# Performance work log

Measured on AMD Instinct MI355X. Metric: run time of the kernel, lower is better.

The kernel has to match this reference:

```python
import jax, jax.numpy as jnp
import numpy as np
from jax import lax

DN = ('NCHW', 'OIHW', 'NCHW')


def _conv_block(x, w, g, b, pool):
    # 3x3 conv (pad 1), BN-inference folded to affine (g, b), ReLU, optional 2x2 maxpool
    x = lax.conv_general_dilated(x, w, (1, 1), 'SAME', dimension_numbers=DN)
    x = jax.nn.relu(x * g[None, :, None, None] + b[None, :, None, None])
    if pool:
        x = lax.reduce_window(x, -jnp.inf, lax.max, (1, 1, 2, 2), (1, 1, 2, 2), 'VALID')
    return x


def _encode(x, w1, g1, b1, w2, g2, b2, w3, g3, b3, w4, g4, b4):
    # Conv64F: pool in blocks 1,2 (84->42->21), no pool in blocks 3,4; then global avg pool
    x = _conv_block(x, w1, g1, b1, True)
    x = _conv_block(x, w2, g2, b2, True)
    x = _conv_block(x, w3, g3, b3, False)
    x = _conv_block(x, w4, g4, b4, False)
    return jnp.mean(x, axis=(2, 3))  # (N, 64)


def setup_inputs() -> dict:
    key = jax.random.key(0)
    ks = jax.random.split(key, 9)
    B, NQ, Way, Shot, C, H, W = 4, 15, 5, 5, 3, 84, 84
    d = {
        'query': jax.random.normal(ks[0], (B, NQ, C, H, W), jnp.float32),
        'support': jax.random.normal(ks[1], (B, Way, Shot, C, H, W), jnp.float32),
        'w1': jax.random.normal(ks[2], (64, 3, 3, 3), jnp.float32) * 0.1,
        'g1': jnp.ones((64,), jnp.float32), 'b1': jnp.zeros((64,), jnp.float32),
        'w2': jax.random.normal(ks[3], (64, 64, 3, 3), jnp.float32) * 0.05,
        'g2': jnp.ones((64,), jnp.float32), 'b2': jnp.zeros((64,), jnp.float32),
        'w3': jax.random.normal(ks[4], (64, 64, 3, 3), jnp.float32) * 0.05,
        'g3': jnp.ones((64,), jnp.float32), 'b3': jnp.zeros((64,), jnp.float32),
        'w4': jax.random.normal(ks[5], (64, 64, 3, 3), jnp.float32) * 0.05,
        'g4': jnp.ones((64,), jnp.float32), 'b4': jnp.zeros((64,), jnp.float32),
        'fc1_w': jax.random.normal(ks[6], (64, 64), jnp.float32) * 0.1,
        'fc1_b': jnp.zeros((64,), jnp.float32),
        'fc2_w': jax.random.normal(ks[7], (32, 64), jnp.float32) * 0.1,
        'fc2_b': jnp.zeros((32,), jnp.float32),
        'fc3_w': jax.random.normal(ks[8], (1, 32), jnp.float32) * 0.1,
        'fc3_b': jnp.zeros((1,), jnp.float32),
    }
    return d


def reference(query, support, w1, g1, b1, w2, g2, b2, w3, g3, b3, w4, g4, b4,
              fc1_w, fc1_b, fc2_w, fc2_b, fc3_w, fc3_b):
    B, NQ, C, H, W = query.shape
    _, Way, Shot = support.shape[:3]
    enc = lambda x: _encode(x, w1, g1, b1, w2, g2, b2, w3, g3, b3, w4, g4, b4)
    q_emb = enc(query.reshape(-1, C, H, W)).reshape(B, NQ, 64)
    s_emb = enc(support.reshape(-1, C, H, W)).reshape(B, Way, Shot, 64)
    # batched pairwise |diff|: (B, NQ, Way, Shot, 64)
    diff = jnp.abs(q_emb[:, :, None, None, :] - s_emb[:, None, :, :, :])
    # relation net (dropout is identity at inference)
    h = jax.nn.relu(jnp.einsum('bqwsd,od->bqwso', diff, fc1_w) + fc1_b)
    h = jax.nn.relu(jnp.einsum('bqwsd,od->bqwso', h, fc2_w) + fc2_b)
    sim = jax.nn.sigmoid(jnp.einsum('bqwsd,od->bqwso', h, fc3_w) + fc3_b)[..., 0]
    scores = jnp.mean(sim, axis=3)  # mean over Shot -> (B, NQ, Way)
    return scores.reshape(B * NQ, Way)
```

## Files before the change

### kernel.cpp

```cpp
#include <hip/hip_runtime.h>
#include <math.h>

typedef unsigned short ushort_t;
typedef __attribute__((ext_vector_type(8))) short bf16x8;
typedef __attribute__((ext_vector_type(16))) float f32x16;

__device__ __forceinline__ ushort_t f2bf(float f) {
    unsigned u = __float_as_uint(f);
    u += 0x7fffu + ((u >> 16) & 1u);
    return (ushort_t)(u >> 16);
}
__device__ __forceinline__ float bf2f(ushort_t h) {
    return __uint_as_float(((unsigned)h) << 16);
}

template <int HP>
__device__ __forceinline__ void zero_halo(ushort_t* buf, int n, int t, int nthr)
{
    const size_t PSTR = (size_t)160 * HP * HP * 32;
    constexpr int W = HP - 2;
    constexpr int NB = 2 * HP + 2 * W;
    for (int j = t; j < 2 * NB; j += nthr) {
        const int pl = j / NB, i = j % NB;
        int yy, xx;
        if (i < HP)            { yy = 0;            xx = i; }
        else if (i < 2 * HP)   { yy = HP - 1;       xx = i - HP; }
        else if (i < 2*HP + W) { yy = i - 2*HP + 1; xx = 0; }
        else                   { yy = i - 2*HP - W + 1; xx = HP - 1; }
        uint4* p = (uint4*)(buf + pl * PSTR +
                            ((size_t)n * HP * HP + yy * HP + xx) * 32);
        const uint4 z = make_uint4(0u, 0u, 0u, 0u);
        p[0] = z; p[1] = z;
    }
}

__global__ __launch_bounds__(256) void prep_k(
    const float* __restrict__ q, const float* __restrict__ s,
    const float* __restrict__ w1, const float* __restrict__ w2,
    const float* __restrict__ w3, const float* __restrict__ w4,
    ushort_t* __restrict__ p0, ushort_t* __restrict__ pw1,
    ushort_t* __restrict__ pw234,
    ushort_t* __restrict__ P1, ushort_t* __restrict__ P2,
    float* __restrict__ embv)
{
    const int b = blockIdx.x, t = threadIdx.x;
    if (b < 160) {
        const int n = b;
        const float* src; int nn;
        if (n < 60) { src = q; nn = n; } else { src = s; nn = n - 60; }
        const float* img = src + (size_t)nn * 3 * 7056;
        for (int px = t; px < 7396; px += 256) {
            const int y = px / 86, x = px % 86;
            uint4 v = make_uint4(0u, 0u, 0u, 0u);
            if (y >= 1 && y <= 84 && x >= 1 && x <= 84) {
                const int o = (y - 1) * 84 + (x - 1);
                const unsigned c0 = f2bf(img[o]);
                const unsigned c1 = f2bf(img[7056 + o]);
                const unsigned c2 = f2bf(img[14112 + o]);
                v.x = c0 | (c1 << 16);
                v.y = c2;
            }
            *(uint4*)(p0 + ((size_t)n * 7396 + px) * 8) = v;
        }
    } else if (b < 167) {
        const int bw = b - 160;
        if (bw == 0) {
            for (int idx = t; idx < 5120; idx += 256) {
                const int sl = idx >> 10, rem = idx & 1023;
                const int co = rem >> 4, c = rem & 15;
                const int h = c >> 3, e = c & 7, tap = 2 * sl + h;
                float v = 0.f;
                if (tap < 9 && e < 3) v = w1[co * 27 + e * 9 + tap];
                pw1[idx] = f2bf(v);
            }
        } else {
            const int l = (bw - 1) >> 1, pass = (bw - 1) & 1;
            const float* w = (l == 0) ? w2 : (l == 1) ? w3 : w4;
            ushort_t* dst = pw234 + l * 36864 + pass * 18432;
            for (int idx = t; idx < 18432; idx += 256) {
                const int c  = idx & 7;
                const int co = (idx >> 3) & 63;
                const int h  = (idx >> 9) & 1;
                const int kl = (idx >> 10) & 1;
                const int tap = idx >> 11;
                const int ci = pass * 32 + kl * 16 + h * 8 + c;
                dst[idx] = f2bf(w[co * 576 + ci * 9 + tap]);
            }
        }
    } else if (b < 327) {
        const int n = b - 167;
        zero_halo<44>(P1, n, t, 256);
        zero_halo<23>(P2, n, t, 256);
    } else {
        for (int i = t; i < 2560; i += 256)
            ((uint4*)embv)[i] = make_uint4(0u, 0u, 0u, 0u);
    }
}

__global__ __launch_bounds__(256, 2) void conv1_lds_k(
    const ushort_t* __restrict__ p0, const ushort_t* __restrict__ pw1,
    const float* __restrict__ gg, const float* __restrict__ bb,
    ushort_t* __restrict__ outp)
{
    constexpr int ROWB = 86 * 16 + 16;
    constexpr int R = 6;
    constexpr int PXB = 84;
    constexpr size_t PLANE1 = (size_t)160 * 1936 * 32;

    __shared__ __align__(16) char alds[R * ROWB];
    __shared__ __align__(16) char blds[10240];

    const int tid = threadIdx.x, wv = tid >> 6, lane = tid & 63;
    const int l31 = lane & 31, h = lane >> 5;
    const int s = blockIdx.x, n = blockIdx.y;
    const int row0 = 4 * s;

    int abase[3];
#pragma unroll
    for (int t = 0; t < 3; ++t) {
        const int ml = wv * 96 + t * 32 + l31;
        int pp = ml >> 2; if (pp > PXB - 1) pp = PXB - 1;
        const int qd = ml & 3;
        const int p = PXB * s + pp;
        const int pr = p / 42, pc = p % 42;
        const int yl = 2 * (pr - 2 * s) + (qd >> 1);
        const int xl = 2 * pc + (qd & 1);
        abase[t] = yl * ROWB + xl * 16;
    }
    int boff[2];
#pragma unroll
    for (int nt = 0; nt < 2; ++nt) boff[nt] = (nt * 32 + l31) * 32 + h * 16;

    {
        const uint4* src = (const uint4*)(p0 + (size_t)n * 7396 * 8);
        for (int i = tid; i < R * 86; i += 256) {
            const int y = i / 86, x = i - y * 86;
            *(uint4*)(alds + y * ROWB + x * 16) = src[(row0 + y) * 86 + x];
        }
    }
    for (int i = tid; i < 640; i += 256)
        ((uint4*)blds)[i] = ((const uint4*)pw1)[i];

    f32x16 acc[3][2];
#pragma unroll
    for (int t = 0; t < 3; ++t)
#pragma unroll
        for (int nt = 0; nt < 2; ++nt)
#pragma unroll
            for (int r = 0; r < 16; ++r) acc[t][nt][r] = 0.f;

    __syncthreads();

#pragma unroll
    for (int st = 0; st < 5; ++st) {
        int tap = 2 * st + h;
        if (tap > 8) tap = 8;
        const int imm = (tap / 3) * ROWB + (tap % 3) * 16;
        const bf16x8 a0 = *(const bf16x8*)(alds + abase[0] + imm);
        const bf16x8 a1 = *(const bf16x8*)(alds + abase[1] + imm);
        const bf16x8 a2 = *(const bf16x8*)(alds + abase[2] + imm);
#pragma unroll
        for (int nt = 0; nt < 2; ++nt) {
            const bf16x8 b = *(const bf16x8*)(blds + st * 2048 + boff[nt]);
            acc[0][nt] = __builtin_amdgcn_mfma_f32_32x32x16_bf16(
                a0, b, acc[0][nt], 0, 0, 0);
            acc[1][nt] = __builtin_amdgcn_mfma_f32_32x32x16_bf16(
                a1, b, acc[1][nt], 0, 0, 0);
            acc[2][nt] = __builtin_amdgcn_mfma_f32_32x32x16_bf16(
                a2, b, acc[2][nt], 0, 0, 0);
        }
    }

    float gv2[2], bv2[2];
#pragma unroll
    for (int nt = 0; nt < 2; ++nt) {
        gv2[nt] = gg[nt * 32 + l31];
        bv2[nt] = bb[nt * 32 + l31];
    }
#pragma unroll
    for (int t = 0; t < 3; ++t) {
#pragma unroll
        for (int g = 0; g < 4; ++g) {
            const int mbase = wv * 96 + t * 32 + 8 * g + 4 * h;
            const int pp = mbase >> 2;
            if (pp >= PXB) continue;
            const int p = PXB * s + pp;
            const int pr = p / 42, pc = p % 42;
            ushort_t* dpix =
                outp + ((size_t)n * 1936 + (pr + 1) * 44 + (pc + 1)) * 32 + l31;
#pragma unroll
            for (int nt = 0; nt < 2; ++nt) {
                float mx = 0.f;
#pragma unroll
                for (int qd = 0; qd < 4; ++qd)
                    mx = fmaxf(mx, fmaf(acc[t][nt][4 * g + qd], gv2[nt], bv2[nt]));
                dpix[nt * PLANE1] = f2bf(mx);
            }
        }
    }
}

__global__ __launch_bounds__(256, 4) void conv2_k(
    const ushort_t* __restrict__ act, const ushort_t* __restrict__ pkw,
    const float* __restrict__ gg, const float* __restrict__ bb,
    ushort_t* __restrict__ outp)
{
    constexpr int HINP = 44, RPB = 3, WAVES = 4, MT = 2;
    constexpr int NTHR = WAVES * 64;
    constexpr int PXB  = 21 * RPB;
    constexpr int R    = 2 * RPB + 2;
    constexpr int ROWB = HINP * 80;
    const size_t APLANE = (size_t)160 * HINP * HINP * 32;
    constexpr size_t OPLANE = (size_t)160 * 529 * 32;

    __shared__ __align__(16) char alds[R * ROWB];

    const int tid = threadIdx.x, wv = tid >> 6, lane = tid & 63;
    const int l31 = lane & 31, h = lane >> 5;
    const int s = blockIdx.x, n = blockIdx.y;
    const int row0 = 2 * RPB * s;

    int abase[MT];
#pragma unroll
    for (int t = 0; t < MT; ++t) {
        const int ml = wv * (MT * 32) + t * 32 + l31;
        int pp = ml >> 2; if (pp > PXB - 1) pp = PXB - 1;
        int p = PXB * s + pp; if (p > 440) p = 440;
        const int qd = ml & 3;
        const int yl = 2 * (p / 21 - RPB * s) + (qd >> 1);
        const int xl = 2 * (p % 21) + (qd & 1);
        abase[t] = yl * ROWB + xl * 80 + h * 16;
    }
    int boff[2];
#pragma unroll
    for (int nt = 0; nt < 2; ++nt) boff[nt] = h * 1024 + (nt * 32 + l31) * 16;

    f32x16 acc[MT][2];
#pragma unroll
    for (int t = 0; t < MT; ++t)
#pragma unroll
        for (int nt = 0; nt < 2; ++nt)
#pragma unroll
            for (int r = 0; r < 16; ++r) acc[t][nt][r] = 0.f;

    bf16x8 br[4][2];

#define B_LD(S, SLOT)                                                      \
    {                                                                      \
        br[SLOT][0] = *(const bf16x8*)(bg + (S)*2048 + boff[0]);           \
        br[SLOT][1] = *(const bf16x8*)(bg + (S)*2048 + boff[1]);           \
    }

    for (int ph = 0; ph < 2; ++ph) {
        const char* bg = (const char*)pkw + ph * 36864;
        B_LD(0, 0) B_LD(1, 1) B_LD(2, 2) B_LD(3, 3)

        if (ph) __syncthreads();
        {
            const uint4* src = (const uint4*)(act +
                (ph * APLANE + (size_t)n * HINP * HINP * 32));
            for (int p = tid; p < R * HINP; p += NTHR) {
                const int y = p / HINP, x = p - y * HINP;
                const int row = min(row0 + y, HINP - 1);
                const uint4* sp = src + ((size_t)row * HINP + x) * 4;
                const uint4 c0 = sp[0], c1 = sp[1], c2 = sp[2], c3 = sp[3];
                char* d = alds + y * ROWB + x * 80;
                *(uint4*)(d)      = c0;
                *(uint4*)(d + 16) = c1;
                *(uint4*)(d + 32) = c2;
                *(uint4*)(d + 48) = c3;
            }
        }
        __syncthreads();

#pragma unroll
        for (int st = 0; st < 18; ++st) {
            const int sl = st & 3;
            const int tap = st >> 1, kl = st & 1;
            const int imm = (tap / 3) * ROWB + (tap % 3) * 80 + kl * 32;
            const bf16x8 a0 = *(const bf16x8*)(alds + abase[0] + imm);
            const bf16x8 a1 = *(const bf16x8*)(alds + abase[1] + imm);
            const bf16x8 b0 = br[sl][0];
            const bf16x8 b1 = br[sl][1];
            if (st < 14) B_LD(st + 4, sl)
            acc[0][0] = __builtin_amdgcn_mfma_f32_32x32x16_bf16(
                a0, b0, acc[0][0], 0, 0, 0);
            acc[1][0] = __builtin_amdgcn_mfma_f32_32x32x16_bf16(
                a1, b0, acc[1][0], 0, 0, 0);
            acc[0][1] = __builtin_amdgcn_mfma_f32_32x32x16_bf16(
                a0, b1, acc[0][1], 0, 0, 0);
            acc[1][1] = __builtin_amdgcn_mfma_f32_32x32x16_bf16(
                a1, b1, acc[1][1], 0, 0, 0);
        }
    }
#undef B_LD

    float gv2[2], bv2[2];
#pragma unroll
    for (int nt = 0; nt < 2; ++nt) {
        gv2[nt] = gg[nt * 32 + l31];
        bv2[nt] = bb[nt * 32 + l31];
    }
#pragma unroll
    for (int t = 0; t < MT; ++t) {
#pragma unroll
        for (int g = 0; g < 4; ++g) {
            const int mbase = wv * (MT * 32) + t * 32 + 8 * g + 4 * h;
            const int pp = mbase >> 2;
            const int p_img = PXB * s + pp;
            if (pp >= PXB || p_img >= 441) continue;
            const int py = p_img / 21, px = p_img % 21;
            ushort_t* dpix = outp +
                ((size_t)n * 529 + (py + 1) * 23 + (px + 1)) * 32 + l31;
#pragma unroll
            for (int nt = 0; nt < 2; ++nt) {
                float mx = 0.f;
#pragma unroll
                for (int qd = 0; qd < 4; ++qd)
                    mx = fmaxf(mx,
                               fmaf(acc[t][nt][4 * g + qd], gv2[nt], bv2[nt]));
                dpix[nt * OPLANE] = f2bf(mx);
            }
        }
    }
}

__global__ __launch_bounds__(512, 2) void conv34_k(
    const ushort_t* __restrict__ P2, const ushort_t* __restrict__ pkw3,
    const ushort_t* __restrict__ pkw4,
    const float* __restrict__ g3, const float* __restrict__ b3,
    const float* __restrict__ g4, const float* __restrict__ b4,
    float* __restrict__ embv)
{
    constexpr int ROWB = 23 * 80;
    constexpr int PLB  = 23 * ROWB;
    const size_t APLANE = (size_t)160 * 529 * 32;

    __shared__ __align__(16) char alds[PLB];
    __shared__ __align__(16) char mid[2 * PLB];

    const int tid = threadIdx.x, wv = tid >> 6, lane = tid & 63;
    const int l31 = lane & 31, h = lane >> 5;
    const int n = blockIdx.x;

    int abase[2];
#pragma unroll
    for (int t = 0; t < 2; ++t) {
        int ml = wv * 64 + t * 32 + l31;
        if (ml > 440) ml = 440;
        abase[t] = (ml / 21) * ROWB + (ml % 21) * 80 + h * 16;
    }
    int boff[2];
#pragma unroll
    for (int nt = 0; nt < 2; ++nt) boff[nt] = h * 1024 + (nt * 32 + l31) * 16;

    f32x16 acc[2][2];
#pragma unroll
    for (int t = 0; t < 2; ++t)
#pragma unroll
        for (int nt = 0; nt < 2; ++nt)
#pragma unroll
            for (int r = 0; r < 16; ++r) acc[t][nt][r] = 0.f;

    bf16x8 br[4][2];

#define B_LD(S, SLOT)                                                      \
    {                                                                      \
        br[SLOT][0] = *(const bf16x8*)(bg + (S)*2048 + boff[0]);           \
        br[SLOT][1] = *(const bf16x8*)(bg + (S)*2048 + boff[1]);           \
    }

    for (int ph = 0; ph < 2; ++ph) {
        const char* bg = (const char*)pkw3 + ph * 36864;
        B_LD(0, 0) B_LD(1, 1) B_LD(2, 2) B_LD(3, 3)

        if (ph) __syncthreads();
        {
            const uint4* src = (const uint4*)(P2 + ph * APLANE +
                                              (size_t)n * 529 * 32);
            for (int p = tid; p < 529; p += 512) {
                const int y = p / 23, x = p - y * 23;
                const uint4* sp = src + (size_t)p * 4;
                const uint4 c0 = sp[0], c1 = sp[1], c2 = sp[2], c3 = sp[3];
                char* d = alds + y * ROWB + x * 80;
                *(uint4*)(d)      = c0;
                *(uint4*)(d + 16) = c1;
                *(uint4*)(d + 32) = c2;
                *(uint4*)(d + 48) = c3;
            }
        }
        __syncthreads();

#pragma unroll
        for (int st = 0; st < 18; ++st) {
            const int sl = st & 3;
            const int tap = st >> 1, kl = st & 1;
            const int imm = (tap / 3) * ROWB + (tap % 3) * 80 + kl * 32;
            const bf16x8 a0 = *(const bf16x8*)(alds + abase[0] + imm);
            const bf16x8 a1 = *(const bf16x8*)(alds + abase[1] + imm);
            const bf16x8 b0 = br[sl][0];
            const bf16x8 b1 = br[sl][1];
            if (st < 14) B_LD(st + 4, sl)
            acc[0][0] = __builtin_amdgcn_mfma_f32_32x32x16_bf16(
                a0, b0, acc[0][0], 0, 0, 0);
            acc[1][0] = __builtin_amdgcn_mfma_f32_32x32x16_bf16(
                a1, b0, acc[1][0], 0, 0, 0);
            acc[0][1] = __builtin_amdgcn_mfma_f32_32x32x16_bf16(
                a0, b1, acc[0][1], 0, 0, 0);
            acc[1][1] = __builtin_amdgcn_mfma_f32_32x32x16_bf16(
                a1, b1, acc[1][1], 0, 0, 0);
        }
    }

    {
        float gv2[2], bv2[2];
#pragma unroll
        for (int nt = 0; nt < 2; ++nt) {
            gv2[nt] = g3[nt * 32 + l31];
            bv2[nt] = b3[nt * 32 + l31];
        }
        for (int j = tid; j < 176; j += 512) {
            const int pl = j / 88, i = j % 88;
            int yy, xx;
            if (i < 23)       { yy = 0;          xx = i; }
            else if (i < 46)  { yy = 22;         xx = i - 23; }
            else if (i < 67)  { yy = i - 46 + 1; xx = 0; }
            else              { yy = i - 67 + 1; xx = 22; }
            char* d = mid + pl * PLB + yy * ROWB + xx * 80;
            const uint4 z = make_uint4(0u, 0u, 0u, 0u);
            *(uint4*)(d)      = z;
            *(uint4*)(d + 16) = z;
            *(uint4*)(d + 32) = z;
            *(uint4*)(d + 48) = z;
        }
#pragma unroll
        for (int t = 0; t < 2; ++t) {
#pragma unroll
            for (int r = 0; r < 16; ++r) {
                const int mloc = wv * 64 + t * 32 + (r & 3) + 8 * (r >> 2) + 4 * h;
                if (mloc >= 441) continue;
                const int y = mloc / 21, x = mloc % 21;
#pragma unroll
                for (int nt = 0; nt < 2; ++nt) {
                    const float v =
                        fmaxf(fmaf(acc[t][nt][r], gv2[nt], bv2[nt]), 0.f);
                    *(ushort_t*)(mid + nt * PLB + (y + 1) * ROWB +
                                 (x + 1) * 80 + l31 * 2) = f2bf(v);
                }
            }
        }
    }
    __syncthreads();

#pragma unroll
    for (int t = 0; t < 2; ++t)
#pragma unroll
        for (int nt = 0; nt < 2; ++nt)
#pragma unroll
            for (int r = 0; r < 16; ++r) acc[t][nt][r] = 0.f;

    for (int ph = 0; ph < 2; ++ph) {
        const char* bg = (const char*)pkw4 + ph * 36864;
        const char* am = mid + ph * PLB;
        B_LD(0, 0) B_LD(1, 1) B_LD(2, 2) B_LD(3, 3)
#pragma unroll
        for (int st = 0; st < 18; ++st) {
            const int sl = st & 3;
            const int tap = st >> 1, kl = st & 1;
            const int imm = (tap / 3) * ROWB + (tap % 3) * 80 + kl * 32;
            const bf16x8 a0 = *(const bf16x8*)(am + abase[0] + imm);
            const bf16x8 a1 = *(const bf16x8*)(am + abase[1] + imm);
            const bf16x8 b0 = br[sl][0];
            const bf16x8 b1 = br[sl][1];
            if (st < 14) B_LD(st + 4, sl)
            acc[0][0] = __builtin_amdgcn_mfma_f32_32x32x16_bf16(
                a0, b0, acc[0][0], 0, 0, 0);
            acc[1][0] = __builtin_amdgcn_mfma_f32_32x32x16_bf16(
                a1, b0, acc[1][0], 0, 0, 0);
            acc[0][1] = __builtin_amdgcn_mfma_f32_32x32x16_bf16(
                a0, b1, acc[0][1], 0, 0, 0);
            acc[1][1] = __builtin_amdgcn_mfma_f32_32x32x16_bf16(
                a1, b1, acc[1][1], 0, 0, 0);
        }
    }
#undef B_LD

    {
        float gv2[2], bv2[2];
#pragma unroll
        for (int nt = 0; nt < 2; ++nt) {
            gv2[nt] = g4[nt * 32 + l31];
            bv2[nt] = b4[nt * 32 + l31];
        }
#pragma unroll
        for (int nt = 0; nt < 2; ++nt) {
            float sum = 0.f;
#pragma unroll
            for (int t = 0; t < 2; ++t) {
#pragma unroll
                for (int r = 0; r < 16; ++r) {
                    const int mloc = wv * 64 + t * 32 +
                                     (r & 3) + 8 * (r >> 2) + 4 * h;
                    if (mloc < 441)
                        sum += fmaxf(fmaf(acc[t][nt][r], gv2[nt], bv2[nt]), 0.f);
                }
            }
            atomicAdd(&embv[(size_t)n * 64 + nt * 32 + l31],
                      sum * (1.f / 441.f));
        }
    }
}

__global__ __launch_bounds__(64) void relation_k(
    const float* __restrict__ emb,
    const float* __restrict__ fc1w, const float* __restrict__ fc1b,
    const float* __restrict__ fc2w, const float* __restrict__ fc2b,
    const float* __restrict__ fc3w, const float* __restrict__ fc3b,
    float* __restrict__ out)
{
    const int idx = blockIdx.x;
    const int w = idx % 5;
    const int bq = idx / 5;
    const int b = bq / 15;
    const int t = threadIdx.x;

    __shared__ float dif[64], h1v[64], h2v[32];
    const float qv = emb[(size_t)bq * 64 + t];

    float ssum = 0.f;
    for (int s = 0; s < 5; ++s) {
        const int simg = 60 + ((b * 5 + w) * 5 + s);
        __syncthreads();
        dif[t] = fabsf(qv - emb[(size_t)simg * 64 + t]);
        __syncthreads();
        float a = fc1b[t];
        for (int d = 0; d < 64; ++d) a = fmaf(fc1w[t * 64 + d], dif[d], a);
        a = fmaxf(a, 0.f);
        __syncthreads();
        h1v[t] = a;
        __syncthreads();
        if (t < 32) {
            float h = fc2b[t];
            for (int d = 0; d < 64; ++d) h = fmaf(fc2w[t * 64 + d], h1v[d], h);
            h2v[t] = fmaxf(h, 0.f);
        }
        __syncthreads();
        float p = (t < 32) ? fc3w[t] * h2v[t] : 0.f;
#pragma unroll
        for (int off = 32; off > 0; off >>= 1) p += __shfl_down(p, off);
        if (t == 0) {
            const float z = p + fc3b[0];
            ssum += 1.f / (1.f + expf(-z));
        }
    }
    if (t == 0) out[idx] = ssum * 0.2f;
}

extern "C" void kernel_launch(void* const* d_in, const int* in_sizes, int n_in,
                              void* d_out, int out_size, void* d_ws, size_t ws_size,
                              hipStream_t stream)
{
    const float* q    = (const float*)d_in[0];
    const float* s    = (const float*)d_in[1];
    const float* w1   = (const float*)d_in[2];
    const float* g1   = (const float*)d_in[3];
    const float* b1p  = (const float*)d_in[4];
    const float* w2   = (const float*)d_in[5];
    const float* g2   = (const float*)d_in[6];
    const float* b2p  = (const float*)d_in[7];
    const float* w3   = (const float*)d_in[8];
    const float* g3   = (const float*)d_in[9];
    const float* b3p  = (const float*)d_in[10];
    const float* w4   = (const float*)d_in[11];
    const float* g4   = (const float*)d_in[12];
    const float* b4p  = (const float*)d_in[13];
    const float* fc1w = (const float*)d_in[14];
    const float* fc1b = (const float*)d_in[15];
    const float* fc2w = (const float*)d_in[16];
    const float* fc2b = (const float*)d_in[17];
    const float* fc3w = (const float*)d_in[18];
    const float* fc3b = (const float*)d_in[19];
    float* out = (float*)d_out;

    char* ws = (char*)d_ws;
    ushort_t* P0    = (ushort_t*)(ws + 0);
    ushort_t* P1    = (ushort_t*)(ws + 18933760);
    ushort_t* P2    = (ushort_t*)(ws + 58583040);
    float*    embv  = (float*)   (ws + 69416960);
    ushort_t* pw1   = (ushort_t*)(ws + 69457920);
    ushort_t* pw234 = (ushort_t*)(ws + 69468160);

    prep_k<<<dim3(328), 256, 0, stream>>>(q, s, w1, w2, w3, w4,
                                          P0, pw1, pw234, P1, P2, embv);

    conv1_lds_k<<<dim3(21, 160), 256, 0, stream>>>(P0, pw1, g1, b1p, P1);

    conv2_k<<<dim3(7, 160), 256, 0, stream>>>(P1, pw234, g2, b2p, P2);

    conv34_k<<<dim3(160), 512, 0, stream>>>(
        P2, pw234 + 36864, pw234 + 2 * 36864, g3, b3p, g4, b4p, embv);

    relation_k<<<dim3(300), 64, 0, stream>>>(
        embv, fc1w, fc1b, fc2w, fc2b, fc3w, fc3b, out);
}
```

Before: 109.3 us.

## Prefetch second channel-half activations into registers during first conv2 K-loop

Conv2 now issues the global loads for the second 32-channel activation plane into registers before running the first half's MFMA loop, then writes them to LDS afterwards. This hides global-load latency for the second phase behind compute. The extra 32 registers per thread led to lowering launch bounds from 4 to 3 blocks per SM, which reduces occupancy.

```diff
diff --git a/kernel.cpp b/kernel.cpp
--- a/kernel.cpp
+++ b/kernel.cpp
@@ -200,7 +200,7 @@
     }
 }
 
-__global__ __launch_bounds__(256, 4) void conv2_k(
+__global__ __launch_bounds__(256, 3) void conv2_k(
     const ushort_t* __restrict__ act, const ushort_t* __restrict__ pkw,
     const float* __restrict__ gg, const float* __restrict__ bb,
     ushort_t* __restrict__ outp)
@@ -210,6 +210,7 @@
     constexpr int PXB  = 21 * RPB;
     constexpr int R    = 2 * RPB + 2;
     constexpr int ROWB = HINP * 80;
+    constexpr int NPIX = R * HINP;
     const size_t APLANE = (size_t)160 * HINP * HINP * 32;
     constexpr size_t OPLANE = (size_t)160 * 529 * 32;
 
@@ -245,54 +246,95 @@
 
     bf16x8 br[4][2];
 
-#define B_LD(S, SLOT)                                                      \
+#define B_LD(BG, S, SLOT)                                                  \
     {                                                                      \
-        br[SLOT][0] = *(const bf16x8*)(bg + (S)*2048 + boff[0]);           \
-        br[SLOT][1] = *(const bf16x8*)(bg + (S)*2048 + boff[1]);           \
-    }
-
-    for (int ph = 0; ph < 2; ++ph) {
-        const char* bg = (const char*)pkw + ph * 36864;
-        B_LD(0, 0) B_LD(1, 1) B_LD(2, 2) B_LD(3, 3)
-
-        if (ph) __syncthreads();
-        {
-            const uint4* src = (const uint4*)(act +
-                (ph * APLANE + (size_t)n * HINP * HINP * 32));
-            for (int p = tid; p < R * HINP; p += NTHR) {
-                const int y = p / HINP, x = p - y * HINP;
-                const int row = min(row0 + y, HINP - 1);
-                const uint4* sp = src + ((size_t)row * HINP + x) * 4;
-                const uint4 c0 = sp[0], c1 = sp[1], c2 = sp[2], c3 = sp[3];
-                char* d = alds + y * ROWB + x * 80;
-                *(uint4*)(d)      = c0;
-                *(uint4*)(d + 16) = c1;
-                *(uint4*)(d + 32) = c2;
-                *(uint4*)(d + 48) = c3;
-            }
-        }
-        __syncthreads();
-
-#pragma unroll
-        for (int st = 0; st < 18; ++st) {
-            const int sl = st & 3;
-            const int tap = st >> 1, kl = st & 1;
-            const int imm = (tap / 3) * ROWB + (tap % 3) * 80 + kl * 32;
-            const bf16x8 a0 = *(const bf16x8*)(alds + abase[0] + imm);
-            const bf16x8 a1 = *(const bf16x8*)(alds + abase[1] + imm);
-            const bf16x8 b0 = br[sl][0];
-            const bf16x8 b1 = br[sl][1];
-            if (st < 14) B_LD(st + 4, sl)
-            acc[0][0] = __builtin_amdgcn_mfma_f32_32x32x16_bf16(
-                a0, b0, acc[0][0], 0, 0, 0);
-            acc[1][0] = __builtin_amdgcn_mfma_f32_32x32x16_bf16(
-                a1, b0, acc[1][0], 0, 0, 0);
-            acc[0][1] = __builtin_amdgcn_mfma_f32_32x32x16_bf16(
-                a0, b1, acc[0][1], 0, 0, 0);
-            acc[1][1] = __builtin_amdgcn_mfma_f32_32x32x16_bf16(
-                a1, b1, acc[1][1], 0, 0, 0);
-        }
-    }
+        br[SLOT][0] = *(const bf16x8*)((BG) + (S)*2048 + boff[0]);         \
+        br[SLOT][1] = *(const bf16x8*)((BG) + (S)*2048 + boff[1]);         \
+    }
+
+#define KLOOP(BG, AL)                                                      \
+    {                                                                      \
+        _Pragma("unroll")                                                  \
+        for (int st = 0; st < 18; ++st) {                                  \
+            const int sl = st & 3;                                         \
+            const int tap = st >> 1, kl = st & 1;                          \
+            const int imm = (tap / 3) * ROWB + (tap % 3) * 80 + kl * 32;   \
+            const bf16x8 a0 = *(const bf16x8*)((AL) + abase[0] + imm);     \
+            const bf16x8 a1 = *(const bf16x8*)((AL) + abase[1] + imm);     \
+            const bf16x8 b0 = br[sl][0];                                   \
+            const bf16x8 b1 = br[sl][1];                                   \
+            if (st < 14) B_LD(BG, st + 4, sl)                              \
+            acc[0][0] = __builtin_amdgcn_mfma_f32_32x32x16_bf16(           \
+                a0, b0, acc[0][0], 0, 0, 0);                               \
+            acc[1][0] = __builtin_amdgcn_mfma_f32_32x32x16_bf16(           \
+                a1, b0, acc[1][0], 0, 0, 0);                               \
+            acc[0][1] = __builtin_amdgcn_mfma_f32_32x32x16_bf16(           \
+                a0, b1, acc[0][1], 0, 0, 0);                               \
+            acc[1][1] = __builtin_amdgcn_mfma_f32_32x32x16_bf16(           \
+                a1, b1, acc[1][1], 0, 0, 0);                               \
+        }                                                                  \
+    }
+
+    const char* bg0 = (const char*)pkw;
+    const char* bg1 = (const char*)pkw + 36864;
+
+    B_LD(bg0, 0, 0) B_LD(bg0, 1, 1) B_LD(bg0, 2, 2) B_LD(bg0, 3, 3)
+    {
+        const uint4* src = (const uint4*)(act + (size_t)n * HINP * HINP * 32);
+        for (int p = tid; p < NPIX; p += NTHR) {
+            const int y = p / HINP, x = p - y * HINP;
+            const int row = min(row0 + y, HINP - 1);
+            const uint4* sp = src + ((size_t)row * HINP + x) * 4;
+            const uint4 c0 = sp[0], c1 = sp[1], c2 = sp[2], c3 = sp[3];
+            char* d = alds + y * ROWB + x * 80;
+            *(uint4*)(d)      = c0;
+            *(uint4*)(d + 16) = c1;
+            *(uint4*)(d + 32) = c2;
+            *(uint4*)(d + 48) = c3;
+        }
+    }
+    __syncthreads();
+
+    uint4 a1buf[2][4];
+    {
+        const uint4* src = (const uint4*)(act + APLANE +
+                                          (size_t)n * HINP * HINP * 32);
+#pragma unroll
+        for (int k = 0; k < 2; ++k) {
+            int p = tid + k * NTHR;
+            if (p >= NPIX) p = 0;
+            const int y = p / HINP, x = p - y * HINP;
+            const int row = min(row0 + y, HINP - 1);
+            const uint4* sp = src + ((size_t)row * HINP + x) * 4;
+            a1buf[k][0] = sp[0];
+            a1buf[k][1] = sp[1];
+            a1buf[k][2] = sp[2];
+            a1buf[k][3] = sp[3];
+        }
+    }
+
+    KLOOP(bg0, alds)
+
+    __syncthreads();
+
+    B_LD(bg1, 0, 0) B_LD(bg1, 1, 1) B_LD(bg1, 2, 2) B_LD(bg1, 3, 3)
+#pragma unroll
+    for (int k = 0; k < 2; ++k) {
+        const int p = tid + k * NTHR;
+        if (p < NPIX) {
+            const int y = p / HINP, x = p - y * HINP;
+            char* d = alds + y * ROWB + x * 80;
+            *(uint4*)(d)      = a1buf[k][0];
+            *(uint4*)(d + 16) = a1buf[k][1];
+            *(uint4*)(d + 32) = a1buf[k][2];
+            *(uint4*)(d + 48) = a1buf[k][3];
+        }
+    }
+    __syncthreads();
+
+    KLOOP(bg1, alds)
+
+#undef KLOOP
 #undef B_LD
 
     float gv2[2], bv2[2];
```

New measurement: 115.8 us. 6.0% more time.
